# Kernel tuning notes

Measured on AMD Instinct MI355X. Metric: run time of the kernel, lower is better.

The kernel has to match this reference:

```python
import jax, jax.numpy as jnp
import numpy as np

D_MODEL = 512
N_HEAD = 8
D_HEAD = D_MODEL // N_HEAD


def setup_inputs() -> dict:
    key = jax.random.key(0)
    ks = jax.random.split(key, 8)
    B, S, T = 4, 512, 32
    src = jax.random.normal(ks[0], (B, S, D_MODEL), dtype=jnp.float32)
    tgt = jax.random.normal(ks[1], (B, S, T, D_MODEL), dtype=jnp.float32)
    tgt_padding_mask = jax.random.bernoulli(ks[2], 0.1, (B, S, T))
    scale = 1.0 / np.sqrt(D_MODEL)
    in_proj_weight = jax.random.uniform(ks[3], (3 * D_MODEL, D_MODEL), dtype=jnp.float32, minval=-scale, maxval=scale)
    in_proj_bias = jnp.zeros((3 * D_MODEL,), dtype=jnp.float32)
    out_proj_weight = jax.random.uniform(ks[4], (D_MODEL, D_MODEL), dtype=jnp.float32, minval=-scale, maxval=scale)
    out_proj_bias = jnp.zeros((D_MODEL,), dtype=jnp.float32)
    return {
        "src": src,
        "tgt": tgt,
        "tgt_padding_mask": tgt_padding_mask,
        "in_proj_weight": in_proj_weight,
        "in_proj_bias": in_proj_bias,
        "out_proj_weight": out_proj_weight,
        "out_proj_bias": out_proj_bias,
    }


def reference(src, tgt, tgt_padding_mask, in_proj_weight, in_proj_bias, out_proj_weight, out_proj_bias):
    # KNN-style cross attention branch (tgt is [B, S, T, D]).
    B, S, _ = src.shape
    T = tgt.shape[-2]
    w_src, w_tgt = in_proj_weight[:D_MODEL], in_proj_weight[D_MODEL:]
    b_src, b_tgt = in_proj_bias[:D_MODEL], in_proj_bias[D_MODEL:]

    q = src @ w_src.T + b_src                      # [B, S, D]
    kv = tgt @ w_tgt.T + b_tgt                     # [B, S, T, 2D]
    k, v = kv[..., :D_MODEL], kv[..., D_MODEL:]

    # mask handling: drop the mask for queries with no valid tgt, zero them later
    attn_invalid = tgt_padding_mask                # [B, S, T]
    mask_no_tgt_valid = jnp.all(attn_invalid, axis=-1)           # [B, S]
    attn_invalid = attn_invalid & ~mask_no_tgt_valid[..., None]

    q = q.reshape(B, S, N_HEAD, D_HEAD)            # [B, S, H, Dh]
    k = k.reshape(B, S, T, N_HEAD, D_HEAD)
    v = v.reshape(B, S, T, N_HEAD, D_HEAD)

    attn = jnp.einsum("bshd,bsthd->bhst", q, k)    # [B, H, S, T]
    attn = jnp.where(attn_invalid[:, None], -jnp.inf, attn)
    attn = jax.nn.softmax(attn / jnp.sqrt(jnp.asarray(D_HEAD, attn.dtype)), axis=-1)

    out = jnp.einsum("bhst,bsthd->bshd", attn, v).reshape(B, S, D_MODEL)
    out = out @ out_proj_weight.T + out_proj_bias
    out = jnp.where(mask_no_tgt_valid[..., None], 0.0, out)
    return out
```

## Files before the change

kernel.cpp:

```cpp
#include <hip/hip_runtime.h>
#include <hip/hip_bf16.h>

#define BS_   2048
#define T_    32
#define DM_   512
#define LDT   520

typedef __attribute__((ext_vector_type(8))) short frag8;
typedef __attribute__((ext_vector_type(4))) float f32x4;

__device__ __forceinline__ short f2s(float v) {
    return __builtin_bit_cast(short, __float2bfloat16(v));
}
__device__ __forceinline__ float s2f(short x) {
    return __builtin_bit_cast(float, (unsigned)(unsigned short)x << 16);
}
__device__ __forceinline__ void stv(float* p, float v)          { *p = v; }
__device__ __forceinline__ void stv(__hip_bfloat16* p, float v) { *p = __float2bfloat16(v); }

__device__ __forceinline__ void gl_lds16(const __hip_bfloat16* g, __hip_bfloat16* l) {
    __builtin_amdgcn_global_load_lds(
        (const __attribute__((address_space(1))) unsigned int*)g,
        (__attribute__((address_space(3))) unsigned int*)l, 16, 0, 0);
}

__global__ __launch_bounds__(256)
void prep(const float* __restrict__ ipw, const float* __restrict__ opw,
          const float* __restrict__ src,
          __hip_bfloat16* __restrict__ ipw_bf, __hip_bfloat16* __restrict__ opw_bf,
          __hip_bfloat16* __restrict__ src_bf, __hip_bfloat16* __restrict__ Tk)
{
    __shared__ __hip_bfloat16 tile[64][65];
    int b = blockIdx.x;
    if (b < 2048) {
        int g = b * 256 + threadIdx.x;
        const float4* in; ushort4* out; int off;
        if (g < 196608)      { in = (const float4*)ipw; out = (ushort4*)ipw_bf; off = g; }
        else if (g < 262144) { in = (const float4*)opw; out = (ushort4*)opw_bf; off = g - 196608; }
        else                 { in = (const float4*)src; out = (ushort4*)src_bf; off = g - 262144; }
        float4 v = in[off];
        ushort4 o;
        o.x = (unsigned short)f2s(v.x); o.y = (unsigned short)f2s(v.y);
        o.z = (unsigned short)f2s(v.z); o.w = (unsigned short)f2s(v.w);
        out[off] = o;
    } else {
        int bb = b - 2048;
        int bx = bb & 15, by = bb >> 4;
        int tid = threadIdx.x;
        const float* sp = ipw + (size_t)512 * 512;
#pragma unroll
        for (int i = 0; i < 16; ++i) {
            int idx = i * 256 + tid;
            int r = idx >> 6, c = idx & 63;
            tile[r][c] = __float2bfloat16(sp[(size_t)(bx * 64 + r) * 512 + by * 64 + c]);
        }
        __syncthreads();
#pragma unroll
        for (int i = 0; i < 16; ++i) {
            int idx = i * 256 + tid;
            int rr = idx >> 6, cc = idx & 63;
            Tk[(size_t)(by * 64 + rr) * 1024 + bx * 64 + cc] = tile[cc][rr];
        }
    }
}

template<typename OUTT>
__global__ __launch_bounds__(256)
void gemm128(const __hip_bfloat16* __restrict__ A,
             const __hip_bfloat16* __restrict__ W,
             const float* __restrict__ bias,
             OUTT* __restrict__ C,
             const int* __restrict__ zrow,
             int M, int N, int K)
{
    __shared__ __hip_bfloat16 sA[128 * 64];
    __shared__ __hip_bfloat16 sB[128 * 64];

    int tid  = threadIdx.x;
    int lane = tid & 63;
    int wave = tid >> 6;
    int tn = blockIdx.x, tm = blockIdx.y;
    int wm = wave >> 1, wn = wave & 1;

    const __hip_bfloat16* Ab = A + (size_t)tm * 128 * K;
    const __hip_bfloat16* Wb = W + (size_t)tn * 128 * K;

    f32x4 acc[4][4];
#pragma unroll
    for (int i = 0; i < 4; ++i)
#pragma unroll
        for (int j = 0; j < 4; ++j) acc[i][j] = {0.f, 0.f, 0.f, 0.f};

    int wbase = (tid & ~63) * 8;
    int m  = lane & 15;
    int q  = lane >> 4;
    int sw = (m & 7) * 8;
    int trow = tid >> 3;
    int tcb  = ((tid & 7) ^ (trow & 7)) * 8;

    for (int k0 = 0; k0 < K; k0 += 64) {
#pragma unroll
        for (int i = 0; i < 4; ++i)
            gl_lds16(Ab + (size_t)(i * 32 + trow) * K + k0 + tcb, &sA[i * 2048 + wbase]);
#pragma unroll
        for (int i = 0; i < 4; ++i)
            gl_lds16(Wb + (size_t)(i * 32 + trow) * K + k0 + tcb, &sB[i * 2048 + wbase]);
        __syncthreads();
#pragma unroll
        for (int ki = 0; ki < 2; ++ki) {
            frag8 af[4], bf[4];
#pragma unroll
            for (int i = 0; i < 4; ++i)
                af[i] = *(const frag8*)&sA[(wm * 64 + i * 16 + m) * 64 + (((ki * 4 + q) * 8) ^ sw)];
#pragma unroll
            for (int j = 0; j < 4; ++j)
                bf[j] = *(const frag8*)&sB[(wn * 64 + j * 16 + m) * 64 + (((ki * 4 + q) * 8) ^ sw)];
#pragma unroll
            for (int i = 0; i < 4; ++i)
#pragma unroll
                for (int j = 0; j < 4; ++j)
                    acc[i][j] = __builtin_amdgcn_mfma_f32_16x16x32_bf16(
                        af[i], bf[j], acc[i][j], 0, 0, 0);
        }
        __syncthreads();
    }

    int rb = (lane >> 4) * 4;
#pragma unroll
    for (int j = 0; j < 4; ++j) {
        int   col = tn * 128 + wn * 64 + j * 16 + m;
        float bv  = bias[col];
#pragma unroll
        for (int i = 0; i < 4; ++i) {
            int row0 = tm * 128 + wm * 64 + i * 16 + rb;
#pragma unroll
            for (int t = 0; t < 4; ++t) {
                int   row = row0 + t;
                float v   = acc[i][j][t] + bv;
                if (zrow && zrow[row]) v = 0.f;
                stv(&C[(size_t)row * N + col], v);
            }
        }
    }
}

__global__ __launch_bounds__(256)
void gemm_bt_g(const __hip_bfloat16* __restrict__ A, int lda, long astr,
               const __hip_bfloat16* __restrict__ W, int ldw, long wstr,
               const float* __restrict__ bias, int bstr,
               __hip_bfloat16* __restrict__ C, int ldc, long cstr,
               int M, int N, int K)
{
    int z = blockIdx.y;
    A += (size_t)z * astr;  W += (size_t)z * wstr;  C += (size_t)z * cstr;
    int bcol0 = z * bstr;

    int wave = blockIdx.x * 4 + (threadIdx.x >> 6);
    int lane = threadIdx.x & 63;
    int ntn  = N / 32;
    int tm = wave / ntn, tn = wave - tm * ntn;
    if (tm * 32 >= M) return;

    int r  = lane & 15;
    int kq = (lane >> 4) << 3;
    const __hip_bfloat16* Ap = A + (size_t)(tm * 32 + r) * lda + kq;
    const __hip_bfloat16* Wp = W + (size_t)(tn * 32 + r) * ldw + kq;

    f32x4 acc[2][2];
#pragma unroll
    for (int i = 0; i < 2; ++i)
#pragma unroll
        for (int j = 0; j < 2; ++j) acc[i][j] = {0.f, 0.f, 0.f, 0.f};

    for (int k0 = 0; k0 < K; k0 += 32) {
        frag8 a[2], b[2];
#pragma unroll
        for (int i = 0; i < 2; ++i) a[i] = *(const frag8*)(Ap + (size_t)i * 16 * lda + k0);
#pragma unroll
        for (int j = 0; j < 2; ++j) b[j] = *(const frag8*)(Wp + (size_t)j * 16 * ldw + k0);
#pragma unroll
        for (int i = 0; i < 2; ++i)
#pragma unroll
            for (int j = 0; j < 2; ++j)
                acc[i][j] = __builtin_amdgcn_mfma_f32_16x16x32_bf16(a[i], b[j], acc[i][j], 0, 0, 0);
    }

    int rb = (lane >> 4) * 4;
#pragma unroll
    for (int j = 0; j < 2; ++j) {
        int   col = tn * 32 + j * 16 + r;
        float bv  = bias ? bias[bcol0 + col] : 0.f;
#pragma unroll
        for (int i = 0; i < 2; ++i) {
            int row0 = tm * 32 + i * 16 + rb;
#pragma unroll
            for (int t = 0; t < 4; ++t)
                C[(size_t)(row0 + t) * ldc + col] =
                    __float2bfloat16(acc[i][j][t] + bv);
        }
    }
}

__global__ __launch_bounds__(256)
void fused_attn(const float* __restrict__ tgt,
                const __hip_bfloat16* __restrict__ qkh,
                const int* __restrict__ mask,
                __hip_bfloat16* __restrict__ tbar,
                int* __restrict__ zrow)
{
    int bs  = blockIdx.x;
    int tid = threadIdx.x;

    __shared__ __hip_bfloat16 sT[32 * LDT];
    __shared__ __hip_bfloat16 sQK[4096];
    __shared__ float sP[8][32];
    __shared__ int   sM[32];

    const float* tg = tgt + (size_t)bs * 32 * 512;
#pragma unroll
    for (int i = 0; i < 16; ++i) {
        int idx = i * 256 + tid;
        int row = idx >> 7, c4 = (idx & 127) * 4;
        float4 v = *(const float4*)(tg + (size_t)row * 512 + c4);
        ushort4 o;
        o.x = (unsigned short)f2s(v.x); o.y = (unsigned short)f2s(v.y);
        o.z = (unsigned short)f2s(v.z); o.w = (unsigned short)f2s(v.w);
        *(ushort4*)&sT[row * LDT + c4] = o;
    }
    const ushort4* qk4 = (const ushort4*)(qkh + (size_t)bs * 4096);
#pragma unroll
    for (int i = 0; i < 4; ++i) {
        int idx = i * 256 + tid;
        ((ushort4*)sQK)[idx] = qk4[idx];
    }
    if (tid < 32) sM[tid] = mask[bs * 32 + tid];
    __syncthreads();

    bool allm = true;
#pragma unroll
    for (int t = 0; t < 32; ++t) allm = allm && (sM[t] != 0);

    int h = tid >> 5, t = tid & 31;
    const __hip_bfloat16* qrow = sQK + h * 512;
    const __hip_bfloat16* trow = &sT[t * LDT];
    int rot = t >> 3;
    float s = 0.f;
#pragma unroll
    for (int c8 = 0; c8 < 64; ++c8) {
        int c = (c8 + rot) & 63;
        frag8 a = *(const frag8*)(trow + c * 8);
        frag8 b = *(const frag8*)(qrow + c * 8);
#pragma unroll
        for (int j = 0; j < 8; ++j) s += s2f(a[j]) * s2f(b[j]);
    }
    s *= 0.125f;
    if (!allm && sM[t]) s = -__builtin_inff();

    float mx = s;
    for (int off = 16; off; off >>= 1) mx = fmaxf(mx, __shfl_xor(mx, off, 32));
    float e = __expf(s - mx);
    float sum = e;
    for (int off = 16; off; off >>= 1) sum += __shfl_xor(sum, off, 32);
    sP[h][t] = e / sum;
    if (tid == 0) zrow[bs] = allm ? 1 : 0;
    __syncthreads();

    int h2 = tid >> 5, j32 = tid & 31, c0 = j32 * 16;
    int rot2 = j32 >> 2;
    float acc[16];
#pragma unroll
    for (int j = 0; j < 16; ++j) acc[j] = 0.f;
#pragma unroll
    for (int tt = 0; tt < 32; ++tt) {
        int tp = (tt + rot2) & 31;
        float p = sP[h2][tp];
        frag8 v1 = *(const frag8*)&sT[tp * LDT + c0];
        frag8 v2 = *(const frag8*)&sT[tp * LDT + c0 + 8];
#pragma unroll
        for (int j = 0; j < 8; ++j) { acc[j] += p * s2f(v1[j]); acc[8 + j] += p * s2f(v2[j]); }
    }
    ushort4 o1, o2, o3, o4;
    o1.x = (unsigned short)f2s(acc[0]);  o1.y = (unsigned short)f2s(acc[1]);
    o1.z = (unsigned short)f2s(acc[2]);  o1.w = (unsigned short)f2s(acc[3]);
    o2.x = (unsigned short)f2s(acc[4]);  o2.y = (unsigned short)f2s(acc[5]);
    o2.z = (unsigned short)f2s(acc[6]);  o2.w = (unsigned short)f2s(acc[7]);
    o3.x = (unsigned short)f2s(acc[8]);  o3.y = (unsigned short)f2s(acc[9]);
    o3.z = (unsigned short)f2s(acc[10]); o3.w = (unsigned short)f2s(acc[11]);
    o4.x = (unsigned short)f2s(acc[12]); o4.y = (unsigned short)f2s(acc[13]);
    o4.z = (unsigned short)f2s(acc[14]); o4.w = (unsigned short)f2s(acc[15]);
    ushort4* dst = (ushort4*)(tbar + (size_t)bs * 4096 + h2 * 512 + c0);
    dst[0] = o1; dst[1] = o2; dst[2] = o3; dst[3] = o4;
}

extern "C" void kernel_launch(void* const* d_in, const int* in_sizes, int n_in,
                              void* d_out, int out_size, void* d_ws, size_t ws_size,
                              hipStream_t stream)
{
    const float* src  = (const float*)d_in[0];
    const float* tgt  = (const float*)d_in[1];
    const int*   mask = (const int*)d_in[2];
    const float* ipw  = (const float*)d_in[3];
    const float* ipb  = (const float*)d_in[4];
    const float* opw  = (const float*)d_in[5];
    const float* opb  = (const float*)d_in[6];
    float*       out  = (float*)d_out;

    char* ws = (char*)d_ws;
    __hip_bfloat16* src_bf = (__hip_bfloat16*)(ws);
    __hip_bfloat16* ipw_bf = (__hip_bfloat16*)(ws + ((size_t)2 << 20));
    __hip_bfloat16* opw_bf = (__hip_bfloat16*)(ws + ((size_t)2 << 20) + 1536 * 512 * 2);
    __hip_bfloat16* q_bf   = (__hip_bfloat16*)(ws + ((size_t)4 << 20));
    __hip_bfloat16* Tk     = (__hip_bfloat16*)(ws + ((size_t)6 << 20));
    __hip_bfloat16* qkh    = (__hip_bfloat16*)(ws + ((size_t)8 << 20));
    __hip_bfloat16* tbar   = (__hip_bfloat16*)(ws + ((size_t)24 << 20));
    __hip_bfloat16* ao_bf  = (__hip_bfloat16*)(ws + ((size_t)40 << 20));
    int*            zrow   = (int*)(ws + ((size_t)42 << 20));

    prep<<<2176, 256, 0, stream>>>(ipw, opw, src, ipw_bf, opw_bf, src_bf, Tk);

    gemm128<__hip_bfloat16><<<dim3(4, 16), 256, 0, stream>>>(
        src_bf, ipw_bf, ipb, q_bf, nullptr, BS_, DM_, DM_);

    gemm_bt_g<<<dim3(256, 8), 256, 0, stream>>>(
        q_bf, 512, 64,  Tk, 1024, 64,  nullptr, 0,
        qkh, 4096, 512,  BS_, 512, 64);

    fused_attn<<<BS_, 256, 0, stream>>>(tgt, qkh, mask, tbar, zrow);

    gemm_bt_g<<<dim3(32, 8), 256, 0, stream>>>(
        tbar, 4096, 512,  ipw_bf + (size_t)1024 * 512, 512, (long)64 * 512,
        ipb + 1024, 64,
        ao_bf, 512, 64,  BS_, 64, 512);

    gemm128<float><<<dim3(4, 16), 256, 0, stream>>>(
        ao_bf, opw_bf, opb, out, zrow, BS_, DM_, DM_);
}
```

Measured before the change: 278.5 us.

## Compute per-query attention scores and weighted sum with bf16 MFMA

Replaces the scalar per-thread dot products and weighted accumulation in the fused attention kernel with 16x16x32 bf16 MFMA instructions. The tgt tile is also transposed in LDS so it can serve as the B operand of the P·V product. Probabilities are split into hi/lo bf16 parts to keep precision, and the output is staged through LDS for coalesced stores. This adds a transpose pass, more LDS footprint and extra syncs, and half the MFMA rows (8 heads padded to 16) are wasted.

```diff
diff --git a/kernel.cpp b/kernel.cpp
--- a/kernel.cpp
+++ b/kernel.cpp
@@ -4,7 +4,6 @@
 #define BS_   2048
 #define T_    32
 #define DM_   512
-#define LDT   520
 
 typedef __attribute__((ext_vector_type(8))) short frag8;
 typedef __attribute__((ext_vector_type(4))) float f32x4;
@@ -208,12 +207,16 @@
                 __hip_bfloat16* __restrict__ tbar,
                 int* __restrict__ zrow)
 {
-    int bs  = blockIdx.x;
-    int tid = threadIdx.x;
-
-    __shared__ __hip_bfloat16 sT[32 * LDT];
-    __shared__ __hip_bfloat16 sQK[4096];
-    __shared__ float sP[8][32];
+    int bs   = blockIdx.x;
+    int tid  = threadIdx.x;
+    int lane = tid & 63;
+    int wv   = tid >> 6;
+    int m    = lane & 15;
+    int g4   = lane >> 4;
+
+    __shared__ short sS[32 * 520];
+    __shared__ short sTT[512 * 32];
+    __shared__ short sQK[8 * 520];
     __shared__ int   sM[32];
 
     const float* tg = tgt + (size_t)bs * 32 * 512;
@@ -225,71 +228,115 @@
         ushort4 o;
         o.x = (unsigned short)f2s(v.x); o.y = (unsigned short)f2s(v.y);
         o.z = (unsigned short)f2s(v.z); o.w = (unsigned short)f2s(v.w);
-        *(ushort4*)&sT[row * LDT + c4] = o;
+        *(ushort4*)&sS[row * 520 + c4] = o;
     }
     const ushort4* qk4 = (const ushort4*)(qkh + (size_t)bs * 4096);
 #pragma unroll
     for (int i = 0; i < 4; ++i) {
-        int idx = i * 256 + tid;
-        ((ushort4*)sQK)[idx] = qk4[idx];
+        int u = i * 256 + tid;
+        int h = u >> 7, c4 = (u & 127) * 4;
+        *(ushort4*)&sQK[h * 520 + c4] = qk4[u];
     }
     if (tid < 32) sM[tid] = mask[bs * 32 + tid];
     __syncthreads();
 
-    bool allm = true;
-#pragma unroll
-    for (int t = 0; t < 32; ++t) allm = allm && (sM[t] != 0);
-
-    int h = tid >> 5, t = tid & 31;
-    const __hip_bfloat16* qrow = sQK + h * 512;
-    const __hip_bfloat16* trow = &sT[t * LDT];
-    int rot = t >> 3;
-    float s = 0.f;
-#pragma unroll
-    for (int c8 = 0; c8 < 64; ++c8) {
-        int c = (c8 + rot) & 63;
-        frag8 a = *(const frag8*)(trow + c * 8);
-        frag8 b = *(const frag8*)(qrow + c * 8);
-#pragma unroll
-        for (int j = 0; j < 8; ++j) s += s2f(a[j]) * s2f(b[j]);
-    }
-    s *= 0.125f;
-    if (!allm && sM[t]) s = -__builtin_inff();
-
-    float mx = s;
-    for (int off = 16; off; off >>= 1) mx = fmaxf(mx, __shfl_xor(mx, off, 32));
-    float e = __expf(s - mx);
-    float sum = e;
-    for (int off = 16; off; off >>= 1) sum += __shfl_xor(sum, off, 32);
-    sP[h][t] = e / sum;
+    {
+        int rot = (tid >> 1) & 7;
+#pragma unroll
+        for (int cc = 0; cc < 2; ++cc) {
+            int c = tid + cc * 256;
+#pragma unroll
+            for (int s = 0; s < 8; ++s) {
+                int t0 = ((s + rot) & 7) * 4;
+                ushort4 o;
+                o.x = (unsigned short)sS[(t0 + 0) * 520 + c];
+                o.y = (unsigned short)sS[(t0 + 1) * 520 + c];
+                o.z = (unsigned short)sS[(t0 + 2) * 520 + c];
+                o.w = (unsigned short)sS[(t0 + 3) * 520 + c];
+                *(ushort4*)&sTT[c * 32 + t0] = o;
+            }
+        }
+    }
+
+    int mk0 = sM[m], mk1 = sM[16 + m];
+    bool allm = __all((mk0 != 0) && (mk1 != 0));
     if (tid == 0) zrow[bs] = allm ? 1 : 0;
+
+    f32x4 acc0 = {0.f,0.f,0.f,0.f}, acc1 = {0.f,0.f,0.f,0.f};
+    {
+        const short* qb  = &sQK[(m & 7) * 520 + g4 * 8];
+        const short* t0p = &sS[m * 520 + g4 * 8];
+        const short* t1p = t0p + 16 * 520;
+#pragma unroll
+        for (int k0 = 0; k0 < 512; k0 += 32) {
+            frag8 af = *(const frag8*)(qb + k0);
+            frag8 b0 = *(const frag8*)(t0p + k0);
+            frag8 b1 = *(const frag8*)(t1p + k0);
+            acc0 = __builtin_amdgcn_mfma_f32_16x16x32_bf16(af, b0, acc0, 0, 0, 0);
+            acc1 = __builtin_amdgcn_mfma_f32_16x16x32_bf16(af, b1, acc1, 0, 0, 0);
+        }
+    }
+
+    float p0v[4], p1v[4];
+#pragma unroll
+    for (int r = 0; r < 4; ++r) {
+        float s0 = acc0[r] * 0.125f, s1 = acc1[r] * 0.125f;
+        if (!allm) {
+            if (mk0) s0 = -__builtin_inff();
+            if (mk1) s1 = -__builtin_inff();
+        }
+        float mx = fmaxf(s0, s1);
+#pragma unroll
+        for (int off = 1; off < 16; off <<= 1) mx = fmaxf(mx, __shfl_xor(mx, off));
+        float e0 = __expf(s0 - mx), e1 = __expf(s1 - mx);
+        float sm = e0 + e1;
+#pragma unroll
+        for (int off = 1; off < 16; off <<= 1) sm += __shfl_xor(sm, off);
+        float inv = 1.f / sm;
+        p0v[r] = e0 * inv; p1v[r] = e1 * inv;
+    }
+
     __syncthreads();
 
-    int h2 = tid >> 5, j32 = tid & 31, c0 = j32 * 16;
-    int rot2 = j32 >> 2;
-    float acc[16];
-#pragma unroll
-    for (int j = 0; j < 16; ++j) acc[j] = 0.f;
-#pragma unroll
-    for (int tt = 0; tt < 32; ++tt) {
-        int tp = (tt + rot2) & 31;
-        float p = sP[h2][tp];
-        frag8 v1 = *(const frag8*)&sT[tp * LDT + c0];
-        frag8 v2 = *(const frag8*)&sT[tp * LDT + c0 + 8];
-#pragma unroll
-        for (int j = 0; j < 8; ++j) { acc[j] += p * s2f(v1[j]); acc[8 + j] += p * s2f(v2[j]); }
-    }
-    ushort4 o1, o2, o3, o4;
-    o1.x = (unsigned short)f2s(acc[0]);  o1.y = (unsigned short)f2s(acc[1]);
-    o1.z = (unsigned short)f2s(acc[2]);  o1.w = (unsigned short)f2s(acc[3]);
-    o2.x = (unsigned short)f2s(acc[4]);  o2.y = (unsigned short)f2s(acc[5]);
-    o2.z = (unsigned short)f2s(acc[6]);  o2.w = (unsigned short)f2s(acc[7]);
-    o3.x = (unsigned short)f2s(acc[8]);  o3.y = (unsigned short)f2s(acc[9]);
-    o3.z = (unsigned short)f2s(acc[10]); o3.w = (unsigned short)f2s(acc[11]);
-    o4.x = (unsigned short)f2s(acc[12]); o4.y = (unsigned short)f2s(acc[13]);
-    o4.z = (unsigned short)f2s(acc[14]); o4.w = (unsigned short)f2s(acc[15]);
-    ushort4* dst = (ushort4*)(tbar + (size_t)bs * 4096 + h2 * 512 + c0);
-    dst[0] = o1; dst[1] = o2; dst[2] = o3; dst[3] = o4;
+    short* sPw = &sQK[0] + wv * 512;
+    if (g4 < 2) {
+#pragma unroll
+        for (int r = 0; r < 4; ++r) {
+            int h = g4 * 4 + r;
+            short h0 = f2s(p0v[r]);
+            short h1 = f2s(p1v[r]);
+            sPw[h * 32 + m]            = h0;
+            sPw[h * 32 + 16 + m]       = h1;
+            sPw[256 + h * 32 + m]      = f2s(p0v[r] - s2f(h0));
+            sPw[256 + h * 32 + 16 + m] = f2s(p1v[r] - s2f(h1));
+        }
+    }
+    __syncthreads();
+
+    frag8 paH = *(const frag8*)(sPw + (m & 7) * 32 + g4 * 8);
+    frag8 paL = *(const frag8*)(sPw + 256 + (m & 7) * 32 + g4 * 8);
+
+    short* sO = &sS[0];
+#pragma unroll
+    for (int ci = 0; ci < 8; ++ci) {
+        int cg = wv * 8 + ci;
+        frag8 vb = *(const frag8*)(&sTT[(cg * 16 + m) * 32 + g4 * 8]);
+        f32x4 d = {0.f,0.f,0.f,0.f};
+        d = __builtin_amdgcn_mfma_f32_16x16x32_bf16(paH, vb, d, 0, 0, 0);
+        d = __builtin_amdgcn_mfma_f32_16x16x32_bf16(paL, vb, d, 0, 0, 0);
+        if (g4 < 2) {
+#pragma unroll
+            for (int r = 0; r < 4; ++r)
+                sO[(g4 * 4 + r) * 512 + cg * 16 + m] = f2s(d[r]);
+        }
+    }
+    __syncthreads();
+
+    ushort4* dst = (ushort4*)(tbar + (size_t)bs * 4096);
+    const ushort4* so4 = (const ushort4*)sO;
+#pragma unroll
+    for (int i = 0; i < 4; ++i)
+        dst[i * 256 + tid] = so4[i * 256 + tid];
 }
 
 extern "C" void kernel_launch(void* const* d_in, const int* in_sizes, int n_in,
```

Result: no change. 273.7 us (-1.7%).
